# Optimization experiments

Hardware: AMD Instinct MI355X
Metric: run time of the kernel (lower is better)

Reference implementation:

```python
import jax, jax.numpy as jnp
import numpy as np

B, S, D = 4, 4096, 1024
EXPAND = 2
D_INNER = EXPAND * D          # 2048
D_CONV = 4
CHUNK = 64
H = 16
DH = D // H                   # 64
EPS = 1e-5


def setup_inputs() -> dict:
    key = jax.random.key(0)
    ks = jax.random.split(key, 10)
    s = 0.02
    return {
        "x": jax.random.normal(ks[0], (B, S, D), jnp.float32),
        "norm_w": jnp.ones((D,), jnp.float32),
        "w_up": jax.random.normal(ks[1], (D, D_INNER), jnp.float32) * s,
        "w_gate": jax.random.normal(ks[2], (D, D_INNER), jnp.float32) * s,
        "w_down": jax.random.normal(ks[3], (D_INNER, D), jnp.float32) * s,
        "conv_w": jax.random.normal(ks[4], (D_INNER, 1, D_CONV), jnp.float32) * s,
        "conv_b": jnp.zeros((D_INNER,), jnp.float32),
        "wq": jax.random.normal(ks[5], (D, D), jnp.float32) * s,
        "wk": jax.random.normal(ks[6], (D, D), jnp.float32) * s,
        "wv": jax.random.normal(ks[7], (D, D), jnp.float32) * s,
        "wo": jax.random.normal(ks[8], (D, D), jnp.float32) * s,
    }


def rmsnorm(x, w):
    var = jnp.mean(jnp.square(x.astype(jnp.float32)), axis=-1, keepdims=True)
    return (x * jax.lax.rsqrt(var + EPS).astype(x.dtype)) * w


def causal_dwconv(x, w, b):
    # x: [B, S, C] -> depthwise causal conv along S
    y = jax.lax.conv_general_dilated(
        x.transpose(0, 2, 1), w,
        window_strides=(1,), padding=[(D_CONV - 1, 0)],
        feature_group_count=D_INNER,
        dimension_numbers=("NCH", "OIH", "NCH"))
    return (y + b[None, :, None]).transpose(0, 2, 1)


def hebbian_memory(h, wq, wk, wv, wo):
    # chunked Hebbian associative memory: M += phi(k)^T v, read y = phi(q) M (+ intra-chunk causal)
    phi = lambda t: jax.nn.elu(t) + 1.0
    q = phi((h @ wq).reshape(B, S, H, DH)) * (DH ** -0.5)
    k = phi((h @ wk).reshape(B, S, H, DH))
    v = (h @ wv).reshape(B, S, H, DH)

    def to_chunks(t):  # [B,S,H,DH] -> [N, B, H, CHUNK, DH]
        return t.reshape(B, S // CHUNK, CHUNK, H, DH).transpose(1, 0, 3, 2, 4)

    qc, kc, vc = to_chunks(q), to_chunks(k), to_chunks(v)
    mask = jnp.tril(jnp.ones((CHUNK, CHUNK), bool))

    def step(M, inp):
        qb, kb, vb = inp                                   # [B,H,C,DH]
        inter = jnp.einsum("bhcd,bhde->bhce", qb, M)       # read from past memory
        sc = jnp.einsum("bhcd,bhed->bhce", qb, kb)
        sc = jnp.where(mask, sc, 0.0)                      # causal intra-chunk Hebbian read
        intra = jnp.einsum("bhce,bhed->bhcd", sc, vb)
        M = M + jnp.einsum("bhcd,bhce->bhde", kb, vb)      # Hebbian outer-product write
        return M, inter + intra

    M0 = jnp.zeros((B, H, DH, DH), h.dtype)
    _, y = jax.lax.scan(step, M0, (qc, kc, vc))            # y: [N,B,H,C,DH]
    y = y.transpose(1, 0, 3, 2, 4).reshape(B, S, D)
    return y @ wo


def reference(x, norm_w, w_up, w_gate, w_down, conv_w, conv_b, wq, wk, wv, wo):
    normed = rmsnorm(x, norm_w)
    val = jax.nn.silu(causal_dwconv(normed @ w_up, conv_w, conv_b))   # conv local mixing
    h = (jax.nn.silu(normed @ w_gate) * val) @ w_down                 # gated MLP
    out = hebbian_memory(h, wq, wk, wv, wo)                           # associative memory
    return x + out
```

## Files before the change

### kernel.cpp

```cpp
#include <hip/hip_runtime.h>
#include <hip/hip_fp16.h>
#include <cstdint>

#define NRALL 16384
#define DM    1024
#define DI    2048
#define SEQL  4096

typedef _Float16 f16;
typedef _Float16 f16x8 __attribute__((ext_vector_type(8)));
typedef _Float16 f16x4 __attribute__((ext_vector_type(4)));
typedef _Float16 f16x2 __attribute__((ext_vector_type(2)));
typedef float    f32x4 __attribute__((ext_vector_type(4)));

__device__ __forceinline__ float phi_f(float t)  { return t > 0.0f ? t + 1.0f : __expf(t); }
__device__ __forceinline__ float silu_f(float t) { return t / (1.0f + __expf(-t)); }

#define GLDS16(g, l)                                                            \
    __builtin_amdgcn_global_load_lds(                                           \
        (const __attribute__((address_space(1))) void*)(g),                     \
        (__attribute__((address_space(3))) void*)(l), 16, 0, 0)

__device__ __forceinline__ void wfmt_one(const float* __restrict__ W, char* __restrict__ fmt,
                                         int n, int kt, int Nw, int Ntot, int noff)
{
    const int ng = noff + n;
#pragma unroll
    for (int kh = 0; kh < 2; ++kh) {
        char* o = fmt + ((size_t)(kt * 2 + kh) * Ntot + ng) * 64;
#pragma unroll
        for (int c2 = 0; c2 < 4; ++c2) {
            f16x8 p;
#pragma unroll
            for (int j = 0; j < 8; ++j)
                p[j] = (f16)W[(size_t)(kt * 64 + kh * 32 + c2 * 8 + j) * Nw + n];
            *(f16x8*)(o + ((c2 ^ ((ng >> 1) & 3)) << 4)) = p;
        }
    }
}

__global__ __launch_bounds__(256) void prep_k(const float* __restrict__ x,
                                              const float* __restrict__ nw,
                                              f16* __restrict__ xn,
                                              const float* __restrict__ w_up,
                                              const float* __restrict__ w_gate,
                                              const float* __restrict__ w_down,
                                              const float* __restrict__ wq,
                                              const float* __restrict__ wk,
                                              const float* __restrict__ wv,
                                              const float* __restrict__ wo,
                                              char* __restrict__ fmtUG,
                                              char* __restrict__ fmtD,
                                              char* __restrict__ fmtQKV,
                                              char* __restrict__ fmtO)
{
    const int t = threadIdx.x;
    if (blockIdx.x < NRALL) {
        const int r = blockIdx.x;
        const float4 v = *(const float4*)(x + (size_t)r * DM + t * 4);
        float s = v.x * v.x + v.y * v.y + v.z * v.z + v.w * v.w;
#pragma unroll
        for (int m = 1; m < 64; m <<= 1) s += __shfl_xor(s, m);
        __shared__ float ws4[4];
        if ((t & 63) == 0) ws4[t >> 6] = s;
        __syncthreads();
        const float tot = ws4[0] + ws4[1] + ws4[2] + ws4[3];
        const float sc = rsqrtf(tot * (1.0f / DM) + 1e-5f);
        const float4 w = *(const float4*)(nw + t * 4);
        f16x4 o;
        o[0] = (f16)(v.x * sc * w.x); o[1] = (f16)(v.y * sc * w.y);
        o[2] = (f16)(v.z * sc * w.z); o[3] = (f16)(v.w * sc * w.w);
        *(f16x4*)(xn + (size_t)r * DM + t * 4) = o;
        return;
    }
    int id = blockIdx.x - NRALL;
    if (id < 128) { wfmt_one(w_up,   fmtUG,  (id % 8) * 256 + t, id / 8, DI, 4096, 0);    return; }
    id -= 128;
    if (id < 128) { wfmt_one(w_gate, fmtUG,  (id % 8) * 256 + t, id / 8, DI, 4096, 2048); return; }
    id -= 128;
    if (id < 128) { wfmt_one(w_down, fmtD,   (id % 4) * 256 + t, id / 4, DM, 1024, 0);    return; }
    id -= 128;
    if (id < 64)  { wfmt_one(wq,     fmtQKV, (id % 4) * 256 + t, id / 4, DM, 3072, 0);    return; }
    id -= 64;
    if (id < 64)  { wfmt_one(wk,     fmtQKV, (id % 4) * 256 + t, id / 4, DM, 3072, 1024); return; }
    id -= 64;
    if (id < 64)  { wfmt_one(wv,     fmtQKV, (id % 4) * 256 + t, id / 4, DM, 3072, 2048); return; }
    id -= 64;
    wfmt_one(wo, fmtO, (id % 4) * 256 + t, id / 4, DM, 1024, 0);
}

#define PH(p, ks, mh, STAGE_STMT)                                                 \
    {                                                                             \
        if ((mh) == 0) {                                                          \
            _Pragma("unroll")                                                     \
            for (int q = 0; q < 2; ++q) {                                         \
                const int row = wm * 64 + q * 16 + lr16;                          \
                af[q] = *(const f16x8*)(ldsb + (p) * 32768 + (ks) * 16384         \
                        + row * 64 + ((kb ^ ((row >> 1) & 3)) << 4));             \
            }                                                                     \
            _Pragma("unroll")                                                     \
            for (int q = 0; q < 4; ++q) {                                         \
                const int n = wn * 64 + q * 16 + lr16;                            \
                bf[q] = *(const f16x8*)(ldsb + 65536 + (p) * 32768 + (ks) * 16384 \
                        + n * 64 + ((kb ^ ((n >> 1) & 3)) << 4));                 \
            }                                                                     \
        } else {                                                                  \
            _Pragma("unroll")                                                     \
            for (int q = 0; q < 2; ++q) {                                         \
                const int row = wm * 64 + (q + 2) * 16 + lr16;                    \
                af[2 + q] = *(const f16x8*)(ldsb + (p) * 32768 + (ks) * 16384     \
                            + row * 64 + ((kb ^ ((row >> 1) & 3)) << 4));         \
            }                                                                     \
        }                                                                         \
        STAGE_STMT;                                                               \
        asm volatile("s_waitcnt vmcnt(3)" ::: "memory");                          \
        __builtin_amdgcn_sched_barrier(0);                                        \
        __builtin_amdgcn_s_barrier();                                             \
        asm volatile("s_waitcnt lgkmcnt(0)" ::: "memory");                        \
        __builtin_amdgcn_sched_barrier(0);                                        \
        __builtin_amdgcn_s_setprio(1);                                            \
        _Pragma("unroll")                                                         \
        for (int q = 0; q < 2; ++q) {                                             \
            acc[(mh) * 2 + q][0] = __builtin_amdgcn_mfma_f32_16x16x32_f16(        \
                af[(mh) * 2 + q], bf[0], acc[(mh) * 2 + q][0], 0, 0, 0);          \
            acc[(mh) * 2 + q][1] = __builtin_amdgcn_mfma_f32_16x16x32_f16(        \
                af[(mh) * 2 + q], bf[1], acc[(mh) * 2 + q][1], 0, 0, 0);          \
            acc[(mh) * 2 + q][2] = __builtin_amdgcn_mfma_f32_16x16x32_f16(        \
                af[(mh) * 2 + q], bf[2], acc[(mh) * 2 + q][2], 0, 0, 0);          \
            acc[(mh) * 2 + q][3] = __builtin_amdgcn_mfma_f32_16x16x32_f16(        \
                af[(mh) * 2 + q], bf[3], acc[(mh) * 2 + q][3], 0, 0, 0);          \
        }                                                                         \
        __builtin_amdgcn_s_setprio(0);                                            \
        __builtin_amdgcn_sched_barrier(0);                                        \
    }

template <int EPI>
__global__ __launch_bounds__(1024) void mg256_k(const f16* __restrict__ A, int lda,
                                                const char* __restrict__ fmt,
                                                void* __restrict__ Cv,
                                                int N, int K, int gx,
                                                const float* __restrict__ addx)
{
    __shared__ __align__(16) char ldsb[131072];

    const int t = threadIdx.x;
    int wid = blockIdx.x;
    { const int cpx = gridDim.x >> 3; wid = (wid & 7) * cpx + (wid >> 3); }
    const int bx = wid % gx, by = wid / gx;
    const int bm = by * 256, bn = bx * 256;
    const int lane = t & 63, wv = t >> 6;
    const int wm = wv >> 2, wn = wv & 3;
    const int kb = lane >> 4, lr16 = lane & 15;
    const int NT = K >> 6;

    f32x4 acc[4][4];
#pragma unroll
    for (int i = 0; i < 4; ++i)
#pragma unroll
        for (int j = 0; j < 4; ++j) acc[i][j] = (f32x4)0.0f;

    const int arow = t >> 2;
    const int ac2 = (t & 3) ^ ((arow >> 1) & 3);
    const f16* Abase = A + (size_t)(bm + arow) * lda + ac2 * 8;
    const char* Bbase = fmt + (size_t)bn * 64 + (size_t)t * 16;
    const size_t BKstep = (size_t)N * 64;
    char* ldsT = ldsb + t * 16;

    auto STAGE_A = [&](int p, int kh, int kt) {
        GLDS16(Abase + kt * 64 + kh * 32, ldsT + p * 32768 + kh * 16384);
    };
    auto STAGE_B = [&](int p, int kh, int kt) {
        GLDS16(Bbase + (size_t)(kt * 2 + kh) * BKstep, ldsT + 65536 + p * 32768 + kh * 16384);
    };

    f16x8 af[4], bf[4];

    const int T1 = NT > 1 ? 1 : 0;
    STAGE_B(0, 0, 0); STAGE_A(0, 0, 0);
    STAGE_B(0, 1, 0); STAGE_A(0, 1, 0);
    STAGE_B(1, 0, T1); STAGE_A(1, 0, T1);
    asm volatile("s_waitcnt vmcnt(4)" ::: "memory");
    __builtin_amdgcn_s_barrier();
    __builtin_amdgcn_sched_barrier(0);

    const int NI = NT >> 1;
    for (int i = 0; i < NI; ++i) {
        const int tA = 2 * i + 1 < NT ? 2 * i + 1 : NT - 1;
        const int tB = 2 * i + 2 < NT ? 2 * i + 2 : NT - 1;
        const int tC = 2 * i + 3 < NT ? 2 * i + 3 : NT - 1;
        PH(0, 0, 0, STAGE_B(1, 1, tA))
        PH(0, 0, 1, STAGE_A(1, 1, tA))
        PH(0, 1, 0, STAGE_B(0, 0, tB))
        PH(0, 1, 1, STAGE_A(0, 0, tB))
        PH(1, 0, 0, STAGE_B(0, 1, tB))
        PH(1, 0, 1, STAGE_A(0, 1, tB))
        PH(1, 1, 0, STAGE_B(1, 0, tC))
        PH(1, 1, 1, STAGE_A(1, 0, tC))
    }
    asm volatile("s_waitcnt vmcnt(0)" ::: "memory");

#pragma unroll
    for (int fm = 0; fm < 4; ++fm) {
        const int row0 = bm + wm * 64 + fm * 16 + kb * 4;
#pragma unroll
        for (int fn = 0; fn < 4; ++fn) {
            const int col = bn + wn * 64 + fn * 16 + lr16;
#pragma unroll
            for (int r = 0; r < 4; ++r) {
                float o = acc[fm][fn][r];
                if (EPI == 1) {
                    if (col < DM) o = phi_f(o) * 0.125f;
                    else if (col < 2 * DM) o = phi_f(o);
                }
                if (EPI == 2) {
                    ((float*)Cv)[(size_t)(row0 + r) * N + col] =
                        o + addx[(size_t)(row0 + r) * N + col];
                } else {
                    ((f16*)Cv)[(size_t)(row0 + r) * N + col] = (f16)o;
                }
            }
        }
    }
}

__global__ __launch_bounds__(256) void conv_gate_k(f16* __restrict__ upg,
                                                   const float* __restrict__ cw,
                                                   const float* __restrict__ cb)
{
    const int r0 = blockIdx.x * 16;
    const int c = threadIdx.x * 8;
    float bias[8];
    {
        const float4 b0 = *(const float4*)(cb + c);
        const float4 b1 = *(const float4*)(cb + c + 4);
        bias[0] = b0.x; bias[1] = b0.y; bias[2] = b0.z; bias[3] = b0.w;
        bias[4] = b1.x; bias[5] = b1.y; bias[6] = b1.z; bias[7] = b1.w;
    }
    float tap[8][4];
#pragma unroll
    for (int j = 0; j < 8; ++j)
        *(float4*)tap[j] = *(const float4*)(cw + (size_t)(c + j) * 4);

    const bool lead = (r0 & (SEQL - 1)) == 0;
    f16x8 w0, w1, w2;
    if (lead) {
        w0 = (f16x8)(f16)0; w1 = (f16x8)(f16)0; w2 = (f16x8)(f16)0;
    } else {
        w0 = *(const f16x8*)(upg + (size_t)(r0 - 3) * 4096 + c);
        w1 = *(const f16x8*)(upg + (size_t)(r0 - 2) * 4096 + c);
        w2 = *(const f16x8*)(upg + (size_t)(r0 - 1) * 4096 + c);
    }
#pragma unroll 4
    for (int i = 0; i < 16; ++i) {
        const size_t row = (size_t)(r0 + i);
        const f16x8 w3 = *(const f16x8*)(upg + row * 4096 + c);
        const f16x8 g  = *(const f16x8*)(upg + row * 4096 + 2048 + c);
        f16x8 o;
#pragma unroll
        for (int j = 0; j < 8; ++j) {
            float a = bias[j];
            a = fmaf((float)w0[j], tap[j][0], a);
            a = fmaf((float)w1[j], tap[j][1], a);
            a = fmaf((float)w2[j], tap[j][2], a);
            a = fmaf((float)w3[j], tap[j][3], a);
            o[j] = (f16)(silu_f((float)g[j]) * silu_f(a));
        }
        *(f16x8*)(upg + row * 4096 + 2048 + c) = o;
        w0 = w1; w1 = w2; w2 = w3;
    }
}

__global__ __launch_bounds__(256) void gscan_g_k(const f16* __restrict__ qkv,
                                                 f16* __restrict__ GT)
{
    __shared__ float Ks[4096];
    __shared__ float Vs[4096];
    const int t = threadIdx.x, ch = blockIdx.x, h = blockIdx.y, b = blockIdx.z;
    const int r = t >> 2, c16 = (t & 3) * 16;
    const f16* kp = qkv + ((size_t)b * SEQL + ch * 64 + r) * 3072 + DM + h * 64 + c16;
#pragma unroll
    for (int i = 0; i < 2; ++i) {
        const f16x8 kv = *(const f16x8*)(kp + 8 * i);
        const f16x8 vv = *(const f16x8*)(kp + DM + 8 * i);
#pragma unroll
        for (int j = 0; j < 8; ++j) {
            Ks[r * 64 + c16 + 8 * i + j] = (float)kv[j];
            Vs[r * 64 + c16 + 8 * i + j] = (float)vv[j];
        }
    }
    __syncthreads();
    const int e4 = (t >> 4) * 4, d4 = (t & 15) * 4;
    float4 ag[4] = {};
#pragma unroll 4
    for (int c = 0; c < 64; ++c) {
        float va[4];
        *(float4*)va = *(const float4*)(Vs + c * 64 + e4);
        const float4 ka = *(const float4*)(Ks + c * 64 + d4);
        ag[0].x = fmaf(va[0], ka.x, ag[0].x); ag[0].y = fmaf(va[0], ka.y, ag[0].y);
        ag[0].z = fmaf(va[0], ka.z, ag[0].z); ag[0].w = fmaf(va[0], ka.w, ag[0].w);
        ag[1].x = fmaf(va[1], ka.x, ag[1].x); ag[1].y = fmaf(va[1], ka.y, ag[1].y);
        ag[1].z = fmaf(va[1], ka.z, ag[1].z); ag[1].w = fmaf(va[1], ka.w, ag[1].w);
        ag[2].x = fmaf(va[2], ka.x, ag[2].x); ag[2].y = fmaf(va[2], ka.y, ag[2].y);
        ag[2].z = fmaf(va[2], ka.z, ag[2].z); ag[2].w = fmaf(va[2], ka.w, ag[2].w);
        ag[3].x = fmaf(va[3], ka.x, ag[3].x); ag[3].y = fmaf(va[3], ka.y, ag[3].y);
        ag[3].z = fmaf(va[3], ka.z, ag[3].z); ag[3].w = fmaf(va[3], ka.w, ag[3].w);
    }
    f16* go = GT + (((size_t)b * 16 + h) * 64 + ch) * 4096 + e4 * 64 + d4;
#pragma unroll
    for (int i = 0; i < 4; ++i) {
        f16x4 o;
        o[0] = (f16)ag[i].x; o[1] = (f16)ag[i].y;
        o[2] = (f16)ag[i].z; o[3] = (f16)ag[i].w;
        *(f16x4*)(go + i * 64) = o;
    }
}

__global__ __launch_bounds__(256) void gprefix_k(f16* __restrict__ G)
{
    const int bh = blockIdx.x >> 3, sl = blockIdx.x & 7;
    f16x2* p = (f16x2*)(G + (size_t)bh * 64 * 4096) + sl * 256 + threadIdx.x;
    float r0 = 0.0f, r1 = 0.0f;
#pragma unroll 4
    for (int ch = 0; ch < 64; ++ch) {
        const f16x2 g = *p;
        f16x2 o; o[0] = (f16)r0; o[1] = (f16)r1;
        *p = o;
        r0 += (float)g[0]; r1 += (float)g[1];
        p += 2048;
    }
}

__global__ __launch_bounds__(256) void gscan_y_k(const f16* __restrict__ qkv,
                                                 const f16* __restrict__ GT,
                                                 f16* __restrict__ y)
{
    __shared__ __align__(16) char lds[40960];
    f16* Qs = (f16*)lds;
    f16* Ks = (f16*)(lds + 8192);
    f16* Ms = (f16*)(lds + 16384);
    f16* Vt = (f16*)(lds + 24576);
    f16* Ss = (f16*)(lds + 32768);

    const int t = threadIdx.x, ch = blockIdx.x, h = blockIdx.y, b = blockIdx.z;
    const int lane = t & 63, w = t >> 6;
    const int kb = lane >> 4, lr16 = lane & 15;

    const int r = t >> 2;
    const int c0 = (t & 3) * 2;
    const int rkey = (r >> 1) & 3;
    const f16* qp = qkv + ((size_t)b * SEQL + ch * 64 + r) * 3072 + h * 64;
    const f16* mp = GT + (((size_t)b * 16 + h) * 64 + ch) * 4096 + r * 64;
#pragma unroll
    for (int cc = 0; cc < 2; ++cc) {
        const int c = c0 + cc;
        const int sw = c ^ rkey;
        const f16x8 qv = *(const f16x8*)(qp + c * 8);
        const f16x8 kv = *(const f16x8*)(qp + DM + c * 8);
        const f16x8 vv = *(const f16x8*)(qp + 2 * DM + c * 8);
        const f16x8 mv = *(const f16x8*)(mp + c * 8);
        *(f16x8*)(Qs + r * 64 + sw * 8) = qv;
        *(f16x8*)(Ks + r * 64 + sw * 8) = kv;
        *(f16x8*)(Ms + r * 64 + sw * 8) = mv;
#pragma unroll
        for (int jj = 0; jj < 8; ++jj) {
            const int j = c * 8 + jj;
            Vt[j * 64 + ((((r >> 3) ^ ((j >> 1) & 3)) << 3) + (r & 7))] = vv[jj];
        }
    }
    __syncthreads();

    f16x8 af[2];
    {
        const int row = w * 16 + lr16;
        const int sz = (row >> 1) & 3;
        af[0] = *(const f16x8*)(Qs + row * 64 + (kb ^ sz) * 8);
        af[1] = *(const f16x8*)(Qs + row * 64 + (4 + (kb ^ sz)) * 8);
    }
    f32x4 accs[4];
#pragma unroll
    for (int te = 0; te < 4; ++te) accs[te] = (f32x4)0.0f;
#pragma unroll
    for (int te = 0; te < 4; ++te) {
        const int er = te * 16 + lr16;
        const int es = (er >> 1) & 3;
        const f16x8 b0 = *(const f16x8*)(Ks + er * 64 + (kb ^ es) * 8);
        const f16x8 b1 = *(const f16x8*)(Ks + er * 64 + (4 + (kb ^ es)) * 8);
        accs[te] = __builtin_amdgcn_mfma_f32_16x16x32_f16(af[0], b0, accs[te], 0, 0, 0);
        accs[te] = __builtin_amdgcn_mfma_f32_16x16x32_f16(af[1], b1, accs[te], 0, 0, 0);
    }
#pragma unroll
    for (int te = 0; te < 4; ++te)
#pragma unroll
        for (int rr = 0; rr < 4; ++rr) {
            const int rc = w * 16 + kb * 4 + rr;
            const int ce = te * 16 + lr16;
            const float v = (ce <= rc) ? accs[te][rr] : 0.0f;
            Ss[rc * 64 + ((((ce >> 3) ^ ((rc >> 1) & 3)) << 3) + (ce & 7))] = (f16)v;
        }
    __syncthreads();

    f16x8 as2[2];
    {
        const int row = w * 16 + lr16;
        const int sz = (row >> 1) & 3;
        as2[0] = *(const f16x8*)(Ss + row * 64 + (kb ^ sz) * 8);
        as2[1] = *(const f16x8*)(Ss + row * 64 + (4 + (kb ^ sz)) * 8);
    }
    f32x4 accy[4];
#pragma unroll
    for (int tj = 0; tj < 4; ++tj) accy[tj] = (f32x4)0.0f;
#pragma unroll
    for (int tj = 0; tj < 4; ++tj) {
        const int jr = tj * 16 + lr16;
        const int js = (jr >> 1) & 3;
        const f16x8 m0 = *(const f16x8*)(Ms + jr * 64 + (kb ^ js) * 8);
        const f16x8 m1 = *(const f16x8*)(Ms + jr * 64 + (4 + (kb ^ js)) * 8);
        const f16x8 v0 = *(const f16x8*)(Vt + jr * 64 + (kb ^ js) * 8);
        const f16x8 v1 = *(const f16x8*)(Vt + jr * 64 + (4 + (kb ^ js)) * 8);
        accy[tj] = __builtin_amdgcn_mfma_f32_16x16x32_f16(af[0],  m0, accy[tj], 0, 0, 0);
        accy[tj] = __builtin_amdgcn_mfma_f32_16x16x32_f16(af[1],  m1, accy[tj], 0, 0, 0);
        accy[tj] = __builtin_amdgcn_mfma_f32_16x16x32_f16(as2[0], v0, accy[tj], 0, 0, 0);
        accy[tj] = __builtin_amdgcn_mfma_f32_16x16x32_f16(as2[1], v1, accy[tj], 0, 0, 0);
    }
    f16* yo = y + ((size_t)b * SEQL + ch * 64) * DM + h * 64;
#pragma unroll
    for (int tj = 0; tj < 4; ++tj)
#pragma unroll
        for (int rr = 0; rr < 4; ++rr) {
            const int rc = w * 16 + kb * 4 + rr;
            yo[(size_t)rc * DM + tj * 16 + lr16] = (f16)accy[tj][rr];
        }
}

extern "C" void kernel_launch(void* const* d_in, const int* in_sizes, int n_in,
                              void* d_out, int out_size, void* d_ws, size_t ws_size,
                              hipStream_t stream)
{
    const float* x      = (const float*)d_in[0];
    const float* norm_w = (const float*)d_in[1];
    const float* w_up   = (const float*)d_in[2];
    const float* w_gate = (const float*)d_in[3];
    const float* w_down = (const float*)d_in[4];
    const float* conv_w = (const float*)d_in[5];
    const float* conv_b = (const float*)d_in[6];
    const float* wq     = (const float*)d_in[7];
    const float* wk     = (const float*)d_in[8];
    const float* wv     = (const float*)d_in[9];
    const float* wo     = (const float*)d_in[10];
    float* out = (float*)d_out;

    const size_t BIG_NEED = 247463936ull;
    const bool big = ws_size >= BIG_NEED;

    if (big) {
        char* p = (char*)d_ws;
        f16* upg = (f16*)p;               p += (size_t)NRALL * 4096 * 2;
        f16* hb  = (f16*)p;               p += (size_t)NRALL * DM * 2;
        char* fmtD   = p;                 p += (size_t)64 * 1024 * 64;
        char* fmtQKV = p;                 p += (size_t)32 * 3072 * 64;
        char* fmtO   = p;                 p += (size_t)32 * 1024 * 64;
        f16* xn = (f16*)p;                p += (size_t)NRALL * DM * 2;
        char* fmtUG  = p;
        f16* G = (f16*)xn;
        f16* qkvb = upg;
        f16* yb   = hb;

        prep_k<<<NRALL + 640, 256, 0, stream>>>(x, norm_w, xn, w_up, w_gate, w_down,
                                                wq, wk, wv, wo, fmtUG, fmtD, fmtQKV, fmtO);

        mg256_k<0><<<16 * 64, 1024, 0, stream>>>(xn, DM, fmtUG, upg, 4096, DM, 16, nullptr);
        conv_gate_k<<<NRALL / 16, 256, 0, stream>>>(upg, conv_w, conv_b);
        mg256_k<0><<<4 * 64, 1024, 0, stream>>>(upg + 2048, 4096, fmtD, hb, 1024, DI, 4, nullptr);
        mg256_k<1><<<12 * 64, 1024, 0, stream>>>(hb, DM, fmtQKV, qkvb, 3072, DM, 12, nullptr);

        gscan_g_k<<<dim3(64, 16, 4), 256, 0, stream>>>(qkvb, G);
        gprefix_k<<<512, 256, 0, stream>>>(G);
        gscan_y_k<<<dim3(64, 16, 4), 256, 0, stream>>>(qkvb, G, yb);

        mg256_k<2><<<4 * 64, 1024, 0, stream>>>(yb, DM, fmtO, out, 1024, DM, 4, x);
    } else {
        char* p = (char*)d_ws;
        f16* xn = (f16*)p;                p += (size_t)NRALL * DM * 2;
        f16* upg = (f16*)p;               p += (size_t)SEQL * 4096 * 2;
        f16* hb  = (f16*)p;               p += (size_t)SEQL * DM * 2;
        f16* G = (f16*)p;                 p += (size_t)16 * 64 * 4096 * 2;
        char* fmtUG  = p;                 p += (size_t)32 * 4096 * 64;
        char* fmtD   = p;                 p += (size_t)64 * 1024 * 64;
        char* fmtQKV = p;                 p += (size_t)32 * 3072 * 64;
        char* fmtO   = p;
        f16* qkvb = upg;
        f16* yb   = hb;

        prep_k<<<NRALL + 640, 256, 0, stream>>>(x, norm_w, xn, w_up, w_gate, w_down,
                                                wq, wk, wv, wo, fmtUG, fmtD, fmtQKV, fmtO);

        for (int b = 0; b < 4; ++b) {
            const f16* xnb = xn + (size_t)b * SEQL * DM;
            mg256_k<0><<<16 * 16, 1024, 0, stream>>>(xnb, DM, fmtUG, upg, 4096, DM, 16, nullptr);
            conv_gate_k<<<SEQL / 16, 256, 0, stream>>>(upg, conv_w, conv_b);
            mg256_k<0><<<4 * 16, 1024, 0, stream>>>(upg + 2048, 4096, fmtD, hb, 1024, DI, 4, nullptr);
            mg256_k<1><<<12 * 16, 1024, 0, stream>>>(hb, DM, fmtQKV, qkvb, 3072, DM, 12, nullptr);
            gscan_g_k<<<dim3(64, 16, 1), 256, 0, stream>>>(qkvb, G);
            gprefix_k<<<128, 256, 0, stream>>>(G);
            gscan_y_k<<<dim3(64, 16, 1), 256, 0, stream>>>(qkvb, G, yb);
            mg256_k<2><<<4 * 16, 1024, 0, stream>>>(yb, DM, fmtO,
                                                    out + (size_t)b * SEQL * DM, 1024, DM, 4,
                                                    x + (size_t)b * SEQL * DM);
        }
    }
}
```

Baseline: 533.2 us.

## Fuse causal depthwise conv and SiLU gate into up/gate GEMM epilogue

Interleaves up and gate weight columns so each 256-column GEMM tile holds 128 matching up/gate channel pairs. A new epilogue stages the tile in LDS and applies the causal depthwise conv, bias and SiLU gating in place, writing only the 2048-wide gated value. A small fixup kernel recomputes the first three rows of each 256-row band from saved tail rows of the neighbouring band. This removes the separate conv_gate kernel and the round trip of the 4096-wide up/gate buffer, at the cost of a heavier GEMM epilogue, an extra small launch and LDS staging.

New measurement: 524.3 us. No clear change (-1.7%).

```diff
diff --git a/kernel.cpp b/kernel.cpp
--- a/kernel.cpp
+++ b/kernel.cpp
@@ -22,9 +22,9 @@
         (__attribute__((address_space(3))) void*)(l), 16, 0, 0)
 
 __device__ __forceinline__ void wfmt_one(const float* __restrict__ W, char* __restrict__ fmt,
-                                         int n, int kt, int Nw, int Ntot, int noff)
-{
-    const int ng = noff + n;
+                                         int n, int kt, int Nw, int Ntot, int mul, int off)
+{
+    const int ng = n * mul + off;
 #pragma unroll
     for (int kh = 0; kh < 2; ++kh) {
         char* o = fmt + ((size_t)(kt * 2 + kh) * Ntot + ng) * 64;
@@ -74,19 +74,19 @@
         return;
     }
     int id = blockIdx.x - NRALL;
-    if (id < 128) { wfmt_one(w_up,   fmtUG,  (id % 8) * 256 + t, id / 8, DI, 4096, 0);    return; }
+    if (id < 128) { wfmt_one(w_up,   fmtUG,  (id % 8) * 256 + t, id / 8, DI, 4096, 2, 0); return; }
     id -= 128;
-    if (id < 128) { wfmt_one(w_gate, fmtUG,  (id % 8) * 256 + t, id / 8, DI, 4096, 2048); return; }
+    if (id < 128) { wfmt_one(w_gate, fmtUG,  (id % 8) * 256 + t, id / 8, DI, 4096, 2, 1); return; }
     id -= 128;
-    if (id < 128) { wfmt_one(w_down, fmtD,   (id % 4) * 256 + t, id / 4, DM, 1024, 0);    return; }
+    if (id < 128) { wfmt_one(w_down, fmtD,   (id % 4) * 256 + t, id / 4, DM, 1024, 1, 0); return; }
     id -= 128;
-    if (id < 64)  { wfmt_one(wq,     fmtQKV, (id % 4) * 256 + t, id / 4, DM, 3072, 0);    return; }
+    if (id < 64)  { wfmt_one(wq,     fmtQKV, (id % 4) * 256 + t, id / 4, DM, 3072, 1, 0);    return; }
     id -= 64;
-    if (id < 64)  { wfmt_one(wk,     fmtQKV, (id % 4) * 256 + t, id / 4, DM, 3072, 1024); return; }
+    if (id < 64)  { wfmt_one(wk,     fmtQKV, (id % 4) * 256 + t, id / 4, DM, 3072, 1, 1024); return; }
     id -= 64;
-    if (id < 64)  { wfmt_one(wv,     fmtQKV, (id % 4) * 256 + t, id / 4, DM, 3072, 2048); return; }
+    if (id < 64)  { wfmt_one(wv,     fmtQKV, (id % 4) * 256 + t, id / 4, DM, 3072, 1, 2048); return; }
     id -= 64;
-    wfmt_one(wo, fmtO, (id % 4) * 256 + t, id / 4, DM, 1024, 0);
+    wfmt_one(wo, fmtO, (id % 4) * 256 + t, id / 4, DM, 1024, 1, 0);
 }
 
 #define PH(p, ks, mh, STAGE_STMT)                                                 \
@@ -139,7 +139,10 @@
                                                 const char* __restrict__ fmt,
                                                 void* __restrict__ Cv,
                                                 int N, int K, int gx,
-                                                const float* __restrict__ addx)
+                                                const float* __restrict__ addx,
+                                                const float* __restrict__ cw = nullptr,
+                                                const float* __restrict__ cb = nullptr,
+                                                f16* __restrict__ tailb = nullptr)
 {
     __shared__ __align__(16) char ldsb[131072];
 
@@ -199,6 +202,62 @@
     }
     asm volatile("s_waitcnt vmcnt(0)" ::: "memory");
 
+    if (EPI == 3) {
+        __syncthreads();
+        f16* upT = (f16*)ldsb;
+        f16* gtT = (f16*)(ldsb + 65536);
+#pragma unroll
+        for (int fm = 0; fm < 4; ++fm) {
+            const int row = wm * 64 + fm * 16 + kb * 4;
+#pragma unroll
+            for (int fn = 0; fn < 4; ++fn) {
+                const int col = wn * 64 + fn * 16 + lr16;
+                f16* dst = (col & 1) ? gtT : upT;
+                const int c = col >> 1;
+#pragma unroll
+                for (int r = 0; r < 4; ++r)
+                    dst[(row + r) * 128 + c] = (f16)acc[fm][fn][r];
+            }
+        }
+        __syncthreads();
+        const int c = t & 127, rg = t >> 7;
+        const int cg = bx * 128 + c;
+        const float4 tp = *(const float4*)(cw + (size_t)cg * 4);
+        const float bias = cb[cg];
+        const int r0 = rg * 32;
+        float w0 = 0.f, w1 = 0.f, w2 = 0.f;
+        if (r0 > 0) {
+            w0 = (float)upT[(r0 - 3) * 128 + c];
+            w1 = (float)upT[(r0 - 2) * 128 + c];
+            w2 = (float)upT[(r0 - 1) * 128 + c];
+        }
+        f16* vout = (f16*)Cv;
+#pragma unroll 8
+        for (int i = 0; i < 32; ++i) {
+            const int r = r0 + i;
+            const float u = (float)upT[r * 128 + c];
+            const float g = (float)gtT[r * 128 + c];
+            float a = bias;
+            a = fmaf(w0, tp.x, a); a = fmaf(w1, tp.y, a);
+            a = fmaf(w2, tp.z, a); a = fmaf(u, tp.w, a);
+            vout[(size_t)(bm + r) * 2048 + cg] = (f16)(silu_f(g) * silu_f(a));
+            w0 = w1; w1 = w2; w2 = u;
+        }
+        const int band = bm >> 8;
+        if (rg == 0) {
+#pragma unroll
+            for (int i = 0; i < 3; ++i) {
+                tailb[((size_t)band * 9 + i) * 2048 + cg]     = upT[i * 128 + c];
+                tailb[((size_t)band * 9 + 6 + i) * 2048 + cg] = gtT[i * 128 + c];
+            }
+        } else if (rg == 7) {
+#pragma unroll
+            for (int i = 0; i < 3; ++i)
+                tailb[((size_t)band * 9 + 3 + i) * 2048 + cg] = upT[(253 + i) * 128 + c];
+        }
+        return;
+    }
+
 #pragma unroll
     for (int fm = 0; fm < 4; ++fm) {
         const int row0 = bm + wm * 64 + fm * 16 + kb * 4;
@@ -223,50 +282,41 @@
     }
 }
 
-__global__ __launch_bounds__(256) void conv_gate_k(f16* __restrict__ upg,
-                                                   const float* __restrict__ cw,
-                                                   const float* __restrict__ cb)
-{
-    const int r0 = blockIdx.x * 16;
-    const int c = threadIdx.x * 8;
-    float bias[8];
-    {
-        const float4 b0 = *(const float4*)(cb + c);
-        const float4 b1 = *(const float4*)(cb + c + 4);
-        bias[0] = b0.x; bias[1] = b0.y; bias[2] = b0.z; bias[3] = b0.w;
-        bias[4] = b1.x; bias[5] = b1.y; bias[6] = b1.z; bias[7] = b1.w;
-    }
-    float tap[8][4];
-#pragma unroll
-    for (int j = 0; j < 8; ++j)
-        *(float4*)tap[j] = *(const float4*)(cw + (size_t)(c + j) * 4);
-
-    const bool lead = (r0 & (SEQL - 1)) == 0;
-    f16x8 w0, w1, w2;
-    if (lead) {
-        w0 = (f16x8)(f16)0; w1 = (f16x8)(f16)0; w2 = (f16x8)(f16)0;
-    } else {
-        w0 = *(const f16x8*)(upg + (size_t)(r0 - 3) * 4096 + c);
-        w1 = *(const f16x8*)(upg + (size_t)(r0 - 2) * 4096 + c);
-        w2 = *(const f16x8*)(upg + (size_t)(r0 - 1) * 4096 + c);
-    }
-#pragma unroll 4
-    for (int i = 0; i < 16; ++i) {
-        const size_t row = (size_t)(r0 + i);
-        const f16x8 w3 = *(const f16x8*)(upg + row * 4096 + c);
-        const f16x8 g  = *(const f16x8*)(upg + row * 4096 + 2048 + c);
+__global__ __launch_bounds__(256) void fixconv_k(const f16* __restrict__ tailb,
+                                                 f16* __restrict__ val,
+                                                 const float* __restrict__ cw,
+                                                 const float* __restrict__ cb)
+{
+    const int b = blockIdx.x;
+    if ((b & 15) == 0) return;
+    const int c0 = threadIdx.x * 8;
+    float um[3][8], u[3][8], g[3][8];
+#pragma unroll
+    for (int i = 0; i < 3; ++i) {
+        const f16x8 a  = *(const f16x8*)(tailb + ((size_t)(b - 1) * 9 + 3 + i) * 2048 + c0);
+        const f16x8 bb = *(const f16x8*)(tailb + ((size_t)b * 9 + i) * 2048 + c0);
+        const f16x8 gg = *(const f16x8*)(tailb + ((size_t)b * 9 + 6 + i) * 2048 + c0);
+#pragma unroll
+        for (int j = 0; j < 8; ++j) {
+            um[i][j] = (float)a[j]; u[i][j] = (float)bb[j]; g[i][j] = (float)gg[j];
+        }
+    }
+#pragma unroll
+    for (int r = 0; r < 3; ++r) {
         f16x8 o;
 #pragma unroll
         for (int j = 0; j < 8; ++j) {
-            float a = bias[j];
-            a = fmaf((float)w0[j], tap[j][0], a);
-            a = fmaf((float)w1[j], tap[j][1], a);
-            a = fmaf((float)w2[j], tap[j][2], a);
-            a = fmaf((float)w3[j], tap[j][3], a);
-            o[j] = (f16)(silu_f((float)g[j]) * silu_f(a));
-        }
-        *(f16x8*)(upg + row * 4096 + 2048 + c) = o;
-        w0 = w1; w1 = w2; w2 = w3;
+            const int cg = c0 + j;
+            const float4 tp = *(const float4*)(cw + (size_t)cg * 4);
+            float a = cb[cg];
+            const float wnd[6] = {um[0][j], um[1][j], um[2][j], u[0][j], u[1][j], u[2][j]};
+            a = fmaf(wnd[r],     tp.x, a);
+            a = fmaf(wnd[r + 1], tp.y, a);
+            a = fmaf(wnd[r + 2], tp.z, a);
+            a = fmaf(wnd[r + 3], tp.w, a);
+            o[j] = (f16)(silu_f(g[r][j]) * silu_f(a));
+        }
+        *(f16x8*)(val + ((size_t)b * 256 + r) * 2048 + c0) = o;
     }
 }
 
@@ -454,23 +504,25 @@
 
     if (big) {
         char* p = (char*)d_ws;
-        f16* upg = (f16*)p;               p += (size_t)NRALL * 4096 * 2;
+        f16* val = (f16*)p;               p += (size_t)NRALL * 2048 * 2;
+        f16* qkvb = (f16*)p;              p += (size_t)NRALL * 3072 * 2;
         f16* hb  = (f16*)p;               p += (size_t)NRALL * DM * 2;
         char* fmtD   = p;                 p += (size_t)64 * 1024 * 64;
         char* fmtQKV = p;                 p += (size_t)32 * 3072 * 64;
         char* fmtO   = p;                 p += (size_t)32 * 1024 * 64;
+        f16* tailb = (f16*)p;             p += (size_t)64 * 9 * 2048 * 2;
         f16* xn = (f16*)p;                p += (size_t)NRALL * DM * 2;
         char* fmtUG  = p;
         f16* G = (f16*)xn;
-        f16* qkvb = upg;
-        f16* yb   = hb;
+        f16* yb = hb;
 
         prep_k<<<NRALL + 640, 256, 0, stream>>>(x, norm_w, xn, w_up, w_gate, w_down,
                                                 wq, wk, wv, wo, fmtUG, fmtD, fmtQKV, fmtO);
 
-        mg256_k<0><<<16 * 64, 1024, 0, stream>>>(xn, DM, fmtUG, upg, 4096, DM, 16, nullptr);
-        conv_gate_k<<<NRALL / 16, 256, 0, stream>>>(upg, conv_w, conv_b);
-        mg256_k<0><<<4 * 64, 1024, 0, stream>>>(upg + 2048, 4096, fmtD, hb, 1024, DI, 4, nullptr);
+        mg256_k<3><<<16 * 64, 1024, 0, stream>>>(xn, DM, fmtUG, val, 4096, DM, 16, nullptr,
+                                                 conv_w, conv_b, tailb);
+        fixconv_k<<<64, 256, 0, stream>>>(tailb, val, conv_w, conv_b);
+        mg256_k<0><<<4 * 64, 1024, 0, stream>>>(val, 2048, fmtD, hb, 1024, DI, 4, nullptr);
         mg256_k<1><<<12 * 64, 1024, 0, stream>>>(hb, DM, fmtQKV, qkvb, 3072, DM, 12, nullptr);
 
         gscan_g_k<<<dim3(64, 16, 4), 256, 0, stream>>>(qkvb, G);
@@ -481,24 +533,26 @@
     } else {
         char* p = (char*)d_ws;
         f16* xn = (f16*)p;                p += (size_t)NRALL * DM * 2;
-        f16* upg = (f16*)p;               p += (size_t)SEQL * 4096 * 2;
+        f16* val = (f16*)p;               p += (size_t)SEQL * 2048 * 2;
+        f16* qkvb = (f16*)p;              p += (size_t)SEQL * 3072 * 2;
         f16* hb  = (f16*)p;               p += (size_t)SEQL * DM * 2;
         f16* G = (f16*)p;                 p += (size_t)16 * 64 * 4096 * 2;
         char* fmtUG  = p;                 p += (size_t)32 * 4096 * 64;
         char* fmtD   = p;                 p += (size_t)64 * 1024 * 64;
         char* fmtQKV = p;                 p += (size_t)32 * 3072 * 64;
-        char* fmtO   = p;
-        f16* qkvb = upg;
-        f16* yb   = hb;
+        char* fmtO   = p;                 p += (size_t)32 * 1024 * 64;
+        f16* tailb = (f16*)p;
+        f16* yb = hb;
 
         prep_k<<<NRALL + 640, 256, 0, stream>>>(x, norm_w, xn, w_up, w_gate, w_down,
                                                 wq, wk, wv, wo, fmtUG, fmtD, fmtQKV, fmtO);
 
         for (int b = 0; b < 4; ++b) {
             const f16* xnb = xn + (size_t)b * SEQL * DM;
-            mg256_k<0><<<16 * 16, 1024, 0, stream>>>(xnb, DM, fmtUG, upg, 4096, DM, 16, nullptr);
-            conv_gate_k<<<SEQL / 16, 256, 0, stream>>>(upg, conv_w, conv_b);
-            mg256_k<0><<<4 * 16, 1024, 0, stream>>>(upg + 2048, 4096, fmtD, hb, 1024, DI, 4, nullptr);
+            mg256_k<3><<<16 * 16, 1024, 0, stream>>>(xnb, DM, fmtUG, val, 4096, DM, 16, nullptr,
+                                                     conv_w, conv_b, tailb);
+            fixconv_k<<<16, 256, 0, stream>>>(tailb, val, conv_w, conv_b);
+            mg256_k<0><<<4 * 16, 1024, 0, stream>>>(val, 2048, fmtD, hb, 1024, DI, 4, nullptr);
             mg256_k<1><<<12 * 16, 1024, 0, stream>>>(hb, DM, fmtQKV, qkvb, 3072, DM, 12, nullptr);
             gscan_g_k<<<dim3(64, 16, 1), 256, 0, stream>>>(qkvb, G);
             gprefix_k<<<128, 256, 0, stream>>>(G);
```
